# Kernel optimization log

Hardware: AMD Instinct MI355X
Metric: run time of the kernel (lower is better)

Reference implementation:

```python
import jax, jax.numpy as jnp
import numpy as np

B, T, D, N, OUT = 1024, 128, 16, 64, 1
STD = 0.02


def setup_inputs() -> dict:
    key = jax.random.key(0)
    ks = jax.random.split(key, 17)
    r = lambda k, s: (jax.random.normal(k, s, dtype=jnp.float32) * STD)
    return {
        'x': jax.random.normal(ks[0], (B, T, D), dtype=jnp.float32),
        'U_j': r(ks[1], (D, 1, N)),
        'W_j': r(ks[2], (D, N, N)),
        'b_j': r(ks[3], (D, N)),
        'Wi_w': r(ks[4], (D * N, D * (N + 1))),
        'Wi_b': r(ks[5], (D * N,)),
        'Wf_w': r(ks[6], (D * N, D * (N + 1))),
        'Wf_b': r(ks[7], (D * N,)),
        'Wo_w': r(ks[8], (D * N, D * (N + 1))),
        'Wo_b': r(ks[9], (D * N,)),
        'F_alpha_n': r(ks[10], (D, N, 1)),
        'F_alpha_n_b': r(ks[11], (D, 1)),
        'F_beta_w': r(ks[12], (1, 2 * N)),
        'F_beta_b': r(ks[13], (1,)),
        'Phi_w': r(ks[14], (OUT, 2 * N)),
        'Phi_b': r(ks[15], (OUT,)),
    }


def reference(x, U_j, W_j, b_j, Wi_w, Wi_b, Wf_w, Wf_b, Wo_w, Wo_b,
              F_alpha_n, F_alpha_n_b, F_beta_w, F_beta_b, Phi_w, Phi_b):
    b = x.shape[0]
    d, n = W_j.shape[0], W_j.shape[1]
    u = U_j[:, 0, :]  # [d, n]

    def step(carry, x_t):  # x_t: [b, d]
        h, c = carry  # h: [b, d, n], c: [b, d*n]
        j = jnp.tanh(jnp.einsum('bdn,dnm->bdm', h, W_j)
                     + x_t[:, :, None] * u + b_j)
        inp = jnp.concatenate([x_t, h.reshape(b, -1)], axis=1)  # [b, d*(n+1)]
        i_t = jax.nn.sigmoid(inp @ Wi_w.T + Wi_b)
        f_t = jax.nn.sigmoid(inp @ Wf_w.T + Wf_b)
        o_t = jax.nn.sigmoid(inp @ Wo_w.T + Wo_b)
        c = c * f_t + i_t * j.reshape(b, -1)
        h = (o_t * jnp.tanh(c)).reshape(b, d, n)
        return (h, c), h

    h0 = jnp.zeros((b, d, n), dtype=x.dtype)
    c0 = jnp.zeros((b, d * n), dtype=x.dtype)
    (h_T, _), outs = jax.lax.scan(step, (h0, c0), jnp.swapaxes(x, 0, 1))
    outputs = jnp.transpose(outs, (1, 0, 2, 3))  # [b, t, d, n]

    # temporal attention per variable
    alphas = jnp.exp(jnp.tanh(
        jnp.einsum('btdn,dnk->btdk', outputs, F_alpha_n) + F_alpha_n_b))
    alphas = alphas / jnp.sum(alphas, axis=1, keepdims=True)
    g_n = jnp.sum(alphas * outputs, axis=1)  # [b, d, n]

    hg = jnp.concatenate([g_n, h_T], axis=2)  # [b, d, 2n]
    mu = hg @ Phi_w.T + Phi_b  # [b, d, out]
    betas = jnp.exp(jnp.tanh(hg @ F_beta_w.T + F_beta_b))  # [b, d, 1]
    betas = betas / jnp.sum(betas, axis=1, keepdims=True)
    return jnp.sum(betas * mu, axis=1)  # [b, out]
```

## Files before the change

### kernel.cpp

```cpp
#include <hip/hip_runtime.h>
#include <hip/hip_bf16.h>


namespace {
constexpr int B_  = 1024;
constexpr int T_  = 128;
constexpr int D_  = 16;
constexpr int DN_ = 1024;
constexpr int NIV = 9;
constexpr int NGR = 144;

constexpr size_t INPBUF   = (size_t)NGR * 1024 * 8 * 2;
constexpr size_t OFF_INP0 = 0;
constexpr size_t OFF_INP1 = INPBUF;
constexpr size_t OFF_FLAGS= 2 * INPBUF;
constexpr size_t OFF_SEH  = OFF_FLAGS + (size_t)16 * 128 * 4;
constexpr size_t OFF_SE   = OFF_SEH + (size_t)B_ * DN_ * 4;
constexpr size_t OFF_HT   = OFF_SE  + (size_t)B_ * D_ * 4;
constexpr size_t OFF_W2   = OFF_HT  + (size_t)B_ * DN_ * 4;
constexpr size_t OFF_WJ2  = OFF_W2  + (size_t)16 * 9 * 24576 * 2;
constexpr size_t ZERO_BYTES = OFF_SEH;
}

typedef __attribute__((ext_vector_type(8))) __bf16 bf8;
typedef __attribute__((ext_vector_type(4))) float  f4;
typedef __attribute__((ext_vector_type(4))) unsigned int u32x4;

__device__ __forceinline__ unsigned short f2bf(float v) {
    unsigned int u = __float_as_uint(v);
    unsigned int r = u + 0x7FFFu + ((u >> 16) & 1u);
    return (unsigned short)(r >> 16);
}
__device__ __forceinline__ float rcpf(float x) { return __builtin_amdgcn_rcpf(x); }
__device__ __forceinline__ float tanhf_fast(float x) {
    x = fminf(fmaxf(x, -15.0f), 15.0f);
    float e = __expf(2.0f * x);
    return (e - 1.0f) * rcpf(e + 1.0f);
}
__device__ __forceinline__ float sigmoidf_fast(float x) {
    return rcpf(1.0f + __expf(-x));
}
__device__ __forceinline__ void gl16(const unsigned short* g, unsigned short* l) {
    __builtin_amdgcn_global_load_lds(
        (const __attribute__((address_space(1))) unsigned int*)g,
        (__attribute__((address_space(3))) unsigned int*)l, 16, 0, 0);
}
__device__ __forceinline__ void gl16c(const unsigned short* g, unsigned short* l) {
    __builtin_amdgcn_global_load_lds(
        (const __attribute__((address_space(1))) unsigned int*)g,
        (__attribute__((address_space(3))) unsigned int*)l, 16, 0, 17);
}
__device__ __forceinline__ void st16c(void* gaddr, u32x4 v) {
    unsigned long long a = (unsigned long long)gaddr;
    asm volatile("global_store_dwordx4 %0, %1, off sc0 sc1"
                 :: "v"(a), "v"(v) : "memory");
}
__device__ __forceinline__ void drain_vmem() {
    asm volatile("s_waitcnt vmcnt(0)" ::: "memory");
}

__global__ __launch_bounds__(256)
void prep_w2(const float* __restrict__ Wi, const float* __restrict__ Wf,
             const float* __restrict__ Wo, unsigned short* __restrict__ W2)
{
    int idx = blockIdx.x * 256 + threadIdx.x;
    if (idx >= 16 * 9 * 16 * 192 * 8) return;
    int e   = idx & 7;
    int t1  = idx >> 3;
    int col = t1 % 192;
    int t2  = t1 / 192;
    int kg  = t2 & 15;
    int t3  = t2 >> 4;
    int iv  = t3 % 9;
    int d   = t3 / 9;
    int kp  = iv * 128 + kg * 8 + e;
    int gate = col >> 6, c = col & 63;
    float v = 0.0f;
    if (kp < 16 || kp >= 128) {
        int k = (kp < 16) ? kp : (16 + (kp - 128));
        const float* W = (gate == 0) ? Wi : (gate == 1) ? Wf : Wo;
        v = W[(size_t)(d * 64 + c) * 1040 + k];
    }
    W2[idx] = f2bf(v);
}

__global__ __launch_bounds__(256)
void prep_misc(const float* __restrict__ Wj, const float* __restrict__ x,
               unsigned short* __restrict__ Wj2, unsigned short* __restrict__ inp0)
{
    int idx = blockIdx.x * 256 + threadIdx.x;
    if (idx < 65536) {
        int e  = idx & 7;
        int m  = (idx >> 3) & 63;
        int kb = (idx >> 9) & 7;
        int d  = idx >> 12;
        int n  = kb * 8 + e;
        Wj2[idx] = f2bf(Wj[((size_t)d * 64 + n) * 64 + m]);
    } else if (idx < 65536 + 16384) {
        int i2   = idx - 65536;
        int feat = i2 & 15;
        int b    = i2 >> 4;
        float v  = x[(size_t)b * (T_ * D_) + feat];
        inp0[(((size_t)(feat >> 3)) * 1024 + b) * 8 + (feat & 7)] = f2bf(v);
    }
}

__global__ __launch_bounds__(512, 1)
void scan_kernel(
    const float* __restrict__ x,
    const float* __restrict__ U_j, const float* __restrict__ b_j,
    const float* __restrict__ Wi_b, const float* __restrict__ Wf_b,
    const float* __restrict__ Wo_b,
    const float* __restrict__ F_an, const float* __restrict__ F_anb,
    const unsigned short* __restrict__ W2, const unsigned short* __restrict__ Wj2,
    unsigned short* __restrict__ inp0, unsigned short* __restrict__ inp1,
    int* __restrict__ flags,
    float* __restrict__ Seh, float* __restrict__ Se, float* __restrict__ hT)
{
    const int d   = blockIdx.x;
    const int bt  = blockIdx.y;
    const int b0  = bt * 64;
    const int tid = threadIdx.x;
    const int wv  = tid >> 6;
    const int cw  = wv & 3;
    const int rw  = wv >> 2;
    const int ln  = tid & 63;
    const int lr  = ln & 15;
    const int lg  = ln >> 4;
    const int coln  = cw * 16 + lr;
    const int rbase = rw * 32;

    __shared__ __align__(16) unsigned char smem[140032];
    unsigned short* a_sb0 = (unsigned short*)smem;
    unsigned short* a_sb1 = (unsigned short*)(smem + 16384);
    unsigned short* w_sb  = (unsigned short*)(smem + 32768);
    unsigned short* wj_s  = (unsigned short*)(smem + 131072);
    float* xd_s = (float*)(smem + 139264);
    float* fa_s = xd_s + 64;
    float* e_s  = xd_s + 128;
    typedef float (*hnrow_t)[66];
    hnrow_t hn_s = (hnrow_t)smem;

    const float uc   = U_j[d * 64 + coln];
    const float bc   = b_j[d * 64 + coln];
    const float bi_c = Wi_b[d * 64 + coln];
    const float bf_c = Wf_b[d * 64 + coln];
    const float bo_c = Wo_b[d * 64 + coln];
    const float fanb = F_anb[d];
    if (tid < 64) fa_s[tid] = F_an[d * 64 + tid];
    gl16(Wj2 + (size_t)d * 4096 + (size_t)wv * 512 + (size_t)ln * 8,
         wj_s + wv * 512);
    const unsigned short* W2d = W2 + (size_t)d * (9 * 24576);
    const int jiv = 1 + (d >> 1);
    const int jgb = (d & 1) * 8;

    float c_r[2][4]   = {};
    float seh_r[2][4] = {};
    float se_r = 0.0f;
    const f4 fz = {0.f, 0.f, 0.f, 0.f};

    for (int t = 0; t < T_; ++t) {
        const unsigned short* cur = (t & 1) ? inp1 : inp0;
        unsigned short*       nxt = (t & 1) ? inp0 : inp1;

        if (tid < 64) xd_s[tid] = x[(size_t)(b0 + tid) * (T_ * D_) + t * D_ + d];
        #pragma unroll
        for (int i = 0; i < 6; ++i) {
            int g = wv * 6 + i;
            gl16(W2d + (size_t)g * 512 + (size_t)ln * 8, w_sb + g * 512);
        }
        if (t > 0) {
            if (tid == 0) {
                while (__hip_atomic_load(&flags[bt * 128 + t], __ATOMIC_RELAXED,
                                         __HIP_MEMORY_SCOPE_AGENT) < 16)
                    __builtin_amdgcn_s_sleep(1);
            }
        }
        __syncthreads();
        #pragma unroll
        for (int i = 0; i < 2; ++i) {
            int g = wv * 2 + i;
            gl16c(cur + ((size_t)g * 1024 + b0 + ln) * 8, a_sb0 + g * 512);
        }
        __syncthreads();

        f4 acc[2][3] = {{fz, fz, fz}, {fz, fz, fz}};
        f4 jacc[2]   = {fz, fz};
        int buf = 0;
        for (int iv = 0; iv < NIV; ++iv) {
            unsigned short* a_cur = buf ? a_sb1 : a_sb0;
            if (iv < NIV - 1) {
                unsigned short* a_nxt = buf ? a_sb0 : a_sb1;
                #pragma unroll
                for (int i = 0; i < 2; ++i) {
                    int g = wv * 2 + i;
                    gl16c(cur + ((size_t)((iv + 1) * 16 + g) * 1024 + b0 + ln) * 8,
                          a_nxt + g * 512);
                }
                const unsigned short* wsrc = W2d + (size_t)(iv + 1) * 24576;
                unsigned short* w_nxt = w_sb + (buf ^ 1) * 24576;
                #pragma unroll
                for (int i = 0; i < 6; ++i) {
                    int g = wv * 6 + i;
                    gl16(wsrc + (size_t)g * 512 + (size_t)ln * 8, w_nxt + g * 512);
                }
            }
            const unsigned short* w_cur = w_sb + buf * 24576;
            #pragma unroll
            for (int ks = 0; ks < 4; ++ks) {
                int kg = ks * 4 + lg;
                bf8 bwg[3];
                #pragma unroll
                for (int g = 0; g < 3; ++g)
                    bwg[g] = *(const bf8*)&w_cur[(kg * 192 + g * 64 + coln) * 8];
                #pragma unroll
                for (int mf = 0; mf < 2; ++mf) {
                    bf8 af = *(const bf8*)&a_cur[kg * 512 + (rbase + mf * 16 + lr) * 8];
                    #pragma unroll
                    for (int g = 0; g < 3; ++g)
                        acc[mf][g] = __builtin_amdgcn_mfma_f32_16x16x32_bf16(
                            af, bwg[g], acc[mf][g], 0, 0, 0);
                }
            }
            if (iv == jiv) {
                #pragma unroll
                for (int ks2 = 0; ks2 < 2; ++ks2) {
                    bf8 bw = *(const bf8*)&wj_s[((ks2 * 4 + lg) * 64 + coln) * 8];
                    #pragma unroll
                    for (int mf = 0; mf < 2; ++mf) {
                        bf8 ah = *(const bf8*)&a_cur[(jgb + ks2 * 4 + lg) * 512
                                                     + (rbase + mf * 16 + lr) * 8];
                        jacc[mf] = __builtin_amdgcn_mfma_f32_16x16x32_bf16(
                            ah, bw, jacc[mf], 0, 0, 0);
                    }
                }
            }
            __syncthreads();
            buf ^= 1;
        }

        float hn_r[2][4];
        #pragma unroll
        for (int mf = 0; mf < 2; ++mf) {
            #pragma unroll
            for (int r = 0; r < 4; ++r) {
                int row = rbase + mf * 16 + lg * 4 + r;
                float jr  = tanhf_fast(jacc[mf][r] + xd_s[row] * uc + bc);
                float iv_ = sigmoidf_fast(acc[mf][0][r] + bi_c);
                float fv  = sigmoidf_fast(acc[mf][1][r] + bf_c);
                float ov  = sigmoidf_fast(acc[mf][2][r] + bo_c);
                float cn  = c_r[mf][r] * fv + iv_ * jr;
                c_r[mf][r] = cn;
                float hn = ov * tanhf_fast(cn);
                hn_r[mf][r] = hn;
                hn_s[row][coln] = hn;
            }
        }
        __syncthreads();

        if (t < T_ - 1) {
            {
                __align__(16) unsigned short pk[8];
                #pragma unroll
                for (int e = 0; e < 8; ++e) pk[e] = f2bf(hn_s[ln][wv * 8 + e]);
                st16c(nxt + ((size_t)(16 + 8 * d + wv) * 1024 + b0 + ln) * 8,
                      *(const u32x4*)pk);
            }
            if (d == 0 && tid < 64) {
                const float* xr = &x[(size_t)(b0 + tid) * (T_ * D_) + (t + 1) * D_];
                __align__(16) unsigned short pk[16];
                #pragma unroll
                for (int f = 0; f < 16; ++f) pk[f] = f2bf(xr[f]);
                st16c(nxt + ((size_t)(b0 + tid)) * 8,        *(const u32x4*)&pk[0]);
                st16c(nxt + ((size_t)1024 + b0 + tid) * 8,   *(const u32x4*)&pk[8]);
            }
            drain_vmem();
            __syncthreads();
            if (tid == 0)
                atomicAdd(&flags[bt * 128 + (t + 1)], 1);
        }

        {
            int br_ = tid >> 3, q = tid & 7;
            float s = 0.0f;
            #pragma unroll
            for (int i2 = 0; i2 < 8; ++i2)
                s += hn_s[br_][q * 8 + i2] * fa_s[q * 8 + i2];
            s += __shfl_xor(s, 1);
            s += __shfl_xor(s, 2);
            s += __shfl_xor(s, 4);
            float e = __expf(tanhf_fast(s + fanb));
            if (q == 0) { e_s[br_] = e; se_r += e; }
        }
        __syncthreads();
        #pragma unroll
        for (int mf = 0; mf < 2; ++mf)
            #pragma unroll
            for (int r = 0; r < 4; ++r)
                seh_r[mf][r] += e_s[rbase + mf * 16 + lg * 4 + r] * hn_r[mf][r];
    }

    {
        int br_ = tid >> 3, q = tid & 7;
        #pragma unroll
        for (int i2 = 0; i2 < 2; ++i2) {
            float4 v;
            v.x = hn_s[br_][q * 8 + i2 * 4 + 0];
            v.y = hn_s[br_][q * 8 + i2 * 4 + 1];
            v.z = hn_s[br_][q * 8 + i2 * 4 + 2];
            v.w = hn_s[br_][q * 8 + i2 * 4 + 3];
            *(float4*)&hT[(size_t)(b0 + br_) * DN_ + d * 64 + q * 8 + i2 * 4] = v;
        }
        if (q == 0) Se[(size_t)(b0 + br_) * D_ + d] = se_r;
    }
    #pragma unroll
    for (int mf = 0; mf < 2; ++mf)
        #pragma unroll
        for (int r = 0; r < 4; ++r) {
            int row = rbase + mf * 16 + lg * 4 + r;
            Seh[((size_t)(b0 + row) * D_ + d) * 64 + coln] = seh_r[mf][r];
        }
}

__global__ __launch_bounds__(64)
void final_kernel(const float* __restrict__ hT,
                  const float* __restrict__ Se, const float* __restrict__ Seh,
                  const float* __restrict__ F_bw, const float* __restrict__ F_bb,
                  const float* __restrict__ Phi_w, const float* __restrict__ Phi_b,
                  float* __restrict__ out)
{
    int b = blockIdx.x;
    int tid = threadIdx.x;
    int d = tid >> 2, q = tid & 3;
    float se_inv = 1.0f / Se[(size_t)b * D_ + d];
    float mu = 0.0f, be = 0.0f;
    #pragma unroll
    for (int i = 0; i < 32; ++i) {
        int k = q * 32 + i;
        float hg = (k < 64) ? Seh[((size_t)b * D_ + d) * 64 + k] * se_inv
                            : hT[(size_t)b * DN_ + d * 64 + (k - 64)];
        mu += hg * Phi_w[k];
        be += hg * F_bw[k];
    }
    mu += __shfl_xor(mu, 1); mu += __shfl_xor(mu, 2);
    be += __shfl_xor(be, 1); be += __shfl_xor(be, 2);
    float mud = mu + Phi_b[0];
    float br  = __expf(tanhf_fast(be + F_bb[0]));
    float num = br * mud, den = br;
    #pragma unroll
    for (int off = 4; off < 64; off <<= 1) {
        num += __shfl_xor(num, off);
        den += __shfl_xor(den, off);
    }
    if (tid == 0) out[b] = num / den;
}

extern "C" void kernel_launch(void* const* d_in, const int* in_sizes, int n_in,
                              void* d_out, int out_size, void* d_ws, size_t ws_size,
                              hipStream_t stream)
{
    (void)in_sizes; (void)n_in; (void)out_size; (void)ws_size;
    const float* x     = (const float*)d_in[0];
    const float* U_j   = (const float*)d_in[1];
    const float* W_j   = (const float*)d_in[2];
    const float* b_j   = (const float*)d_in[3];
    const float* Wi_w  = (const float*)d_in[4];
    const float* Wi_b  = (const float*)d_in[5];
    const float* Wf_w  = (const float*)d_in[6];
    const float* Wf_b  = (const float*)d_in[7];
    const float* Wo_w  = (const float*)d_in[8];
    const float* Wo_b  = (const float*)d_in[9];
    const float* F_an  = (const float*)d_in[10];
    const float* F_anb = (const float*)d_in[11];
    const float* F_bw  = (const float*)d_in[12];
    const float* F_bb  = (const float*)d_in[13];
    const float* Phi_w = (const float*)d_in[14];
    const float* Phi_b = (const float*)d_in[15];
    float* out = (float*)d_out;

    char* ws = (char*)d_ws;
    unsigned short* inp0 = (unsigned short*)(ws + OFF_INP0);
    unsigned short* inp1 = (unsigned short*)(ws + OFF_INP1);
    int*   flags = (int*)(ws + OFF_FLAGS);
    float* Seh   = (float*)(ws + OFF_SEH);
    float* Se    = (float*)(ws + OFF_SE);
    float* hT    = (float*)(ws + OFF_HT);
    unsigned short* W2  = (unsigned short*)(ws + OFF_W2);
    unsigned short* Wj2 = (unsigned short*)(ws + OFF_WJ2);

    (void)hipMemsetAsync(d_ws, 0, ZERO_BYTES, stream);
    prep_w2<<<dim3(13824), dim3(256), 0, stream>>>(Wi_w, Wf_w, Wo_w, W2);
    prep_misc<<<dim3(320), dim3(256), 0, stream>>>(W_j, x, Wj2, inp0);

    scan_kernel<<<dim3(16, 16), dim3(512), 0, stream>>>(
        x, U_j, b_j, Wi_b, Wf_b, Wo_b, F_an, F_anb,
        W2, Wj2, inp0, inp1, flags, Seh, Se, hT);

    final_kernel<<<dim3(B_), dim3(64), 0, stream>>>(hT, Se, Seh, F_bw, F_bb,
                                                    Phi_w, Phi_b, out);
}
```

Measured before the change: 1.424 ms.

## Split x-input gate contribution into local MFMA, drop padded x chunk from exchange buffer

Removes the x features from the shared inter-block exchange buffer, which had been padded to a full 128-wide K chunk (mostly zeros). Each block now loads its own x slice into LDS and does a separate small MFMA against a dedicated x-weight tile, so the main K loop runs 8 chunks instead of 9. The block-to-grid mapping is also reordered to a 1D grid that interleaves feature indices. The cost is extra LDS, per-step x loads into LDS, and one more prep pass for the x weights.

```diff
diff --git a/kernel.cpp b/kernel.cpp
--- a/kernel.cpp
+++ b/kernel.cpp
@@ -7,10 +7,9 @@
 constexpr int T_  = 128;
 constexpr int D_  = 16;
 constexpr int DN_ = 1024;
-constexpr int NIV = 9;
-constexpr int NGR = 144;
-
-constexpr size_t INPBUF   = (size_t)NGR * 1024 * 8 * 2;
+constexpr int NIV = 8;
+
+constexpr size_t INPBUF   = (size_t)128 * 1024 * 8 * 2;
 constexpr size_t OFF_INP0 = 0;
 constexpr size_t OFF_INP1 = INPBUF;
 constexpr size_t OFF_FLAGS= 2 * INPBUF;
@@ -18,7 +17,8 @@
 constexpr size_t OFF_SE   = OFF_SEH + (size_t)B_ * DN_ * 4;
 constexpr size_t OFF_HT   = OFF_SE  + (size_t)B_ * D_ * 4;
 constexpr size_t OFF_W2   = OFF_HT  + (size_t)B_ * DN_ * 4;
-constexpr size_t OFF_WJ2  = OFF_W2  + (size_t)16 * 9 * 24576 * 2;
+constexpr size_t OFF_WJ2  = OFF_W2  + (size_t)16 * 8 * 24576 * 2;
+constexpr size_t OFF_WX2  = OFF_WJ2 + (size_t)16 * 4096 * 2;
 constexpr size_t ZERO_BYTES = OFF_SEH;
 }
 
@@ -64,29 +64,26 @@
              const float* __restrict__ Wo, unsigned short* __restrict__ W2)
 {
     int idx = blockIdx.x * 256 + threadIdx.x;
-    if (idx >= 16 * 9 * 16 * 192 * 8) return;
+    if (idx >= 16 * 8 * 16 * 192 * 8) return;
     int e   = idx & 7;
     int t1  = idx >> 3;
     int col = t1 % 192;
     int t2  = t1 / 192;
     int kg  = t2 & 15;
     int t3  = t2 >> 4;
-    int iv  = t3 % 9;
-    int d   = t3 / 9;
-    int kp  = iv * 128 + kg * 8 + e;
+    int iv  = t3 & 7;
+    int d   = t3 >> 3;
+    int k   = 16 + iv * 128 + kg * 8 + e;
     int gate = col >> 6, c = col & 63;
-    float v = 0.0f;
-    if (kp < 16 || kp >= 128) {
-        int k = (kp < 16) ? kp : (16 + (kp - 128));
-        const float* W = (gate == 0) ? Wi : (gate == 1) ? Wf : Wo;
-        v = W[(size_t)(d * 64 + c) * 1040 + k];
-    }
-    W2[idx] = f2bf(v);
+    const float* W = (gate == 0) ? Wi : (gate == 1) ? Wf : Wo;
+    W2[idx] = f2bf(W[(size_t)(d * 64 + c) * 1040 + k]);
 }
 
 __global__ __launch_bounds__(256)
-void prep_misc(const float* __restrict__ Wj, const float* __restrict__ x,
-               unsigned short* __restrict__ Wj2, unsigned short* __restrict__ inp0)
+void prep_misc(const float* __restrict__ Wj,
+               const float* __restrict__ Wi, const float* __restrict__ Wf,
+               const float* __restrict__ Wo,
+               unsigned short* __restrict__ Wj2, unsigned short* __restrict__ Wx2)
 {
     int idx = blockIdx.x * 256 + threadIdx.x;
     if (idx < 65536) {
@@ -96,12 +93,22 @@
         int d  = idx >> 12;
         int n  = kb * 8 + e;
         Wj2[idx] = f2bf(Wj[((size_t)d * 64 + n) * 64 + m]);
-    } else if (idx < 65536 + 16384) {
-        int i2   = idx - 65536;
-        int feat = i2 & 15;
-        int b    = i2 >> 4;
-        float v  = x[(size_t)b * (T_ * D_) + feat];
-        inp0[(((size_t)(feat >> 3)) * 1024 + b) * 8 + (feat & 7)] = f2bf(v);
+    } else if (idx < 65536 + 98304) {
+        int i2  = idx - 65536;
+        int e   = i2 & 7;
+        int t1  = i2 >> 3;
+        int col = t1 % 192;
+        int t2  = t1 / 192;
+        int kg  = t2 & 3;
+        int d   = t2 >> 2;
+        int k   = kg * 8 + e;
+        int gate = col >> 6, c = col & 63;
+        float v = 0.0f;
+        if (k < 16) {
+            const float* W = (gate == 0) ? Wi : (gate == 1) ? Wf : Wo;
+            v = W[(size_t)(d * 64 + c) * 1040 + k];
+        }
+        Wx2[i2] = f2bf(v);
     }
 }
 
@@ -113,12 +120,14 @@
     const float* __restrict__ Wo_b,
     const float* __restrict__ F_an, const float* __restrict__ F_anb,
     const unsigned short* __restrict__ W2, const unsigned short* __restrict__ Wj2,
+    const unsigned short* __restrict__ Wx2,
     unsigned short* __restrict__ inp0, unsigned short* __restrict__ inp1,
     int* __restrict__ flags,
     float* __restrict__ Seh, float* __restrict__ Se, float* __restrict__ hT)
 {
-    const int d   = blockIdx.x;
-    const int bt  = blockIdx.y;
+    const int id  = blockIdx.x;
+    const int d   = (id & 7) * 2 + ((id >> 3) & 1);
+    const int bt  = id >> 4;
     const int b0  = bt * 64;
     const int tid = threadIdx.x;
     const int wv  = tid >> 6;
@@ -130,12 +139,14 @@
     const int coln  = cw * 16 + lr;
     const int rbase = rw * 32;
 
-    __shared__ __align__(16) unsigned char smem[140032];
+    __shared__ __align__(16) unsigned char smem[156416];
     unsigned short* a_sb0 = (unsigned short*)smem;
     unsigned short* a_sb1 = (unsigned short*)(smem + 16384);
     unsigned short* w_sb  = (unsigned short*)(smem + 32768);
     unsigned short* wj_s  = (unsigned short*)(smem + 131072);
-    float* xd_s = (float*)(smem + 139264);
+    unsigned short* wx_s  = (unsigned short*)(smem + 139264);
+    unsigned short* xa_s  = (unsigned short*)(smem + 151552);
+    float* xd_s = (float*)(smem + 155648);
     float* fa_s = xd_s + 64;
     float* e_s  = xd_s + 128;
     typedef float (*hnrow_t)[66];
@@ -148,10 +159,16 @@
     const float bo_c = Wo_b[d * 64 + coln];
     const float fanb = F_anb[d];
     if (tid < 64) fa_s[tid] = F_an[d * 64 + tid];
-    gl16(Wj2 + (size_t)d * 4096 + (size_t)wv * 512 + (size_t)ln * 8,
-         wj_s + wv * 512);
-    const unsigned short* W2d = W2 + (size_t)d * (9 * 24576);
-    const int jiv = 1 + (d >> 1);
+    gl16(Wj2 + (size_t)d * 4096 + (size_t)(wv * 64 + ln) * 8, wj_s + wv * 512);
+    #pragma unroll
+    for (int i = 0; i < 2; ++i) {
+        int g = wv + i * 8;
+        if (g < 12)
+            gl16(Wx2 + (size_t)d * 6144 + (size_t)(g * 64 + ln) * 8, wx_s + g * 512);
+    }
+    *(ushort4*)&xa_s[tid * 4] = make_ushort4(0, 0, 0, 0);
+    const unsigned short* W2d = W2 + (size_t)d * (8 * 24576);
+    const int jiv = d >> 1;
     const int jgb = (d & 1) * 8;
 
     float c_r[2][4]   = {};
@@ -163,11 +180,17 @@
         const unsigned short* cur = (t & 1) ? inp1 : inp0;
         unsigned short*       nxt = (t & 1) ? inp0 : inp1;
 
-        if (tid < 64) xd_s[tid] = x[(size_t)(b0 + tid) * (T_ * D_) + t * D_ + d];
+        if (tid < 64) xd_s[tid] = x[(size_t)(b0 + tid) * 2048 + t * 16 + d];
+        if (tid < 256) {
+            int b = tid >> 2, q = tid & 3;
+            float4 xv = *(const float4*)&x[(size_t)(b0 + b) * 2048 + t * 16 + q * 4];
+            *(ushort4*)&xa_s[b * 32 + q * 4] =
+                make_ushort4(f2bf(xv.x), f2bf(xv.y), f2bf(xv.z), f2bf(xv.w));
+        }
         #pragma unroll
         for (int i = 0; i < 6; ++i) {
-            int g = wv * 6 + i;
-            gl16(W2d + (size_t)g * 512 + (size_t)ln * 8, w_sb + g * 512);
+            int gw = wv * 6 + i;
+            gl16(W2d + (size_t)(gw * 64 + ln) * 8, w_sb + gw * 512);
         }
         if (t > 0) {
             if (tid == 0) {
@@ -177,15 +200,30 @@
             }
         }
         __syncthreads();
+
         #pragma unroll
         for (int i = 0; i < 2; ++i) {
-            int g = wv * 2 + i;
-            gl16c(cur + ((size_t)g * 1024 + b0 + ln) * 8, a_sb0 + g * 512);
-        }
+            int ga = wv * 2 + i;
+            gl16c(cur + ((size_t)ga * 1024 + b0 + ln) * 8, a_sb0 + ga * 512);
+        }
+        f4 acc[2][3];
+        {
+            bf8 wxg[3];
+            #pragma unroll
+            for (int g = 0; g < 3; ++g)
+                wxg[g] = *(const bf8*)&wx_s[(lg * 192 + g * 64 + coln) * 8];
+            #pragma unroll
+            for (int mf = 0; mf < 2; ++mf) {
+                bf8 xa = *(const bf8*)&xa_s[(rbase + mf * 16 + lr) * 32 + lg * 8];
+                #pragma unroll
+                for (int g = 0; g < 3; ++g)
+                    acc[mf][g] = __builtin_amdgcn_mfma_f32_16x16x32_bf16(
+                        xa, wxg[g], fz, 0, 0, 0);
+            }
+        }
+        f4 jacc[2] = {fz, fz};
         __syncthreads();
 
-        f4 acc[2][3] = {{fz, fz, fz}, {fz, fz, fz}};
-        f4 jacc[2]   = {fz, fz};
         int buf = 0;
         for (int iv = 0; iv < NIV; ++iv) {
             unsigned short* a_cur = buf ? a_sb1 : a_sb0;
@@ -193,16 +231,16 @@
                 unsigned short* a_nxt = buf ? a_sb0 : a_sb1;
                 #pragma unroll
                 for (int i = 0; i < 2; ++i) {
-                    int g = wv * 2 + i;
-                    gl16c(cur + ((size_t)((iv + 1) * 16 + g) * 1024 + b0 + ln) * 8,
-                          a_nxt + g * 512);
+                    int ga = wv * 2 + i;
+                    gl16c(cur + ((size_t)((iv + 1) * 16 + ga) * 1024 + b0 + ln) * 8,
+                          a_nxt + ga * 512);
                 }
                 const unsigned short* wsrc = W2d + (size_t)(iv + 1) * 24576;
                 unsigned short* w_nxt = w_sb + (buf ^ 1) * 24576;
                 #pragma unroll
                 for (int i = 0; i < 6; ++i) {
-                    int g = wv * 6 + i;
-                    gl16(wsrc + (size_t)g * 512 + (size_t)ln * 8, w_nxt + g * 512);
+                    int gw = wv * 6 + i;
+                    gl16(wsrc + (size_t)(gw * 64 + ln) * 8, w_nxt + gw * 512);
                 }
             }
             const unsigned short* w_cur = w_sb + buf * 24576;
@@ -259,21 +297,11 @@
         __syncthreads();
 
         if (t < T_ - 1) {
-            {
-                __align__(16) unsigned short pk[8];
-                #pragma unroll
-                for (int e = 0; e < 8; ++e) pk[e] = f2bf(hn_s[ln][wv * 8 + e]);
-                st16c(nxt + ((size_t)(16 + 8 * d + wv) * 1024 + b0 + ln) * 8,
-                      *(const u32x4*)pk);
-            }
-            if (d == 0 && tid < 64) {
-                const float* xr = &x[(size_t)(b0 + tid) * (T_ * D_) + (t + 1) * D_];
-                __align__(16) unsigned short pk[16];
-                #pragma unroll
-                for (int f = 0; f < 16; ++f) pk[f] = f2bf(xr[f]);
-                st16c(nxt + ((size_t)(b0 + tid)) * 8,        *(const u32x4*)&pk[0]);
-                st16c(nxt + ((size_t)1024 + b0 + tid) * 8,   *(const u32x4*)&pk[8]);
-            }
+            __align__(16) unsigned short pk[8];
+            #pragma unroll
+            for (int e = 0; e < 8; ++e) pk[e] = f2bf(hn_s[ln][wv * 8 + e]);
+            st16c(nxt + ((size_t)(d * 8 + wv) * 1024 + b0 + ln) * 8,
+                  *(const u32x4*)pk);
             drain_vmem();
             __syncthreads();
             if (tid == 0)
@@ -387,14 +415,15 @@
     float* hT    = (float*)(ws + OFF_HT);
     unsigned short* W2  = (unsigned short*)(ws + OFF_W2);
     unsigned short* Wj2 = (unsigned short*)(ws + OFF_WJ2);
+    unsigned short* Wx2 = (unsigned short*)(ws + OFF_WX2);
 
     (void)hipMemsetAsync(d_ws, 0, ZERO_BYTES, stream);
-    prep_w2<<<dim3(13824), dim3(256), 0, stream>>>(Wi_w, Wf_w, Wo_w, W2);
-    prep_misc<<<dim3(320), dim3(256), 0, stream>>>(W_j, x, Wj2, inp0);
-
-    scan_kernel<<<dim3(16, 16), dim3(512), 0, stream>>>(
+    prep_w2<<<dim3(12288), dim3(256), 0, stream>>>(Wi_w, Wf_w, Wo_w, W2);
+    prep_misc<<<dim3(640), dim3(256), 0, stream>>>(W_j, Wi_w, Wf_w, Wo_w, Wj2, Wx2);
+
+    scan_kernel<<<dim3(256), dim3(512), 0, stream>>>(
         x, U_j, b_j, Wi_b, Wf_b, Wo_b, F_an, F_anb,
-        W2, Wj2, inp0, inp1, flags, Seh, Se, hT);
+        W2, Wj2, Wx2, inp0, inp1, flags, Seh, Se, hT);
 
     final_kernel<<<dim3(B_), dim3(64), 0, stream>>>(hT, Se, Seh, F_bw, F_bb,
                                                     Phi_w, Phi_b, out);
```

After: 1.370 ms. -3.8%, faster.
